# Optimization experiments

Measured on AMD Instinct MI355X. Metric: run time of the kernel, lower is better.

## Reference

```python
import jax, jax.numpy as jnp
import numpy as np

C_M, C_Z, H, C_HID = 256, 128, 8, 32
N_SEQ, N_RES = 64, 384
INF = 1e9
EPS = 1e-5


def layernorm(x, w, b):
    mu = jnp.mean(x, axis=-1, keepdims=True)
    var = jnp.mean(jnp.square(x - mu), axis=-1, keepdims=True)
    return (x - mu) * jax.lax.rsqrt(var + EPS) * w + b


def setup_inputs() -> dict:
    key = jax.random.key(0)
    ks = jax.random.split(key, 6)
    m = jax.random.normal(ks[0], (N_SEQ, N_RES, C_M), dtype=jnp.float32)
    z = jax.random.normal(ks[1], (N_RES, N_RES, C_Z), dtype=jnp.float32)
    mask = jnp.ones((N_SEQ, N_RES), dtype=jnp.float32)
    return {
        "m": m,
        "z": z,
        "mask": mask,
        "ln_m_w": jnp.ones((C_M,), jnp.float32),
        "ln_m_b": jnp.zeros((C_M,), jnp.float32),
        "ln_z_w": jnp.ones((C_Z,), jnp.float32),
        "ln_z_b": jnp.zeros((C_Z,), jnp.float32),
        "W_z": jax.random.normal(ks[2], (C_Z, H), jnp.float32) * 0.05,
        "W_v": jax.random.normal(ks[3], (C_M, H * C_HID), jnp.float32) * 0.05,
        "W_g": jax.random.normal(ks[4], (C_M, H * C_HID), jnp.float32) * 0.05,
        "W_o": jax.random.normal(ks[5], (H * C_HID, C_M), jnp.float32) * 0.05,
    }


def reference(m, z, mask, ln_m_w, ln_m_b, ln_z_w, ln_z_b, W_z, W_v, W_g, W_o):
    S, N = m.shape[0], m.shape[1]
    # mask: max over MSA rows, keepdim -> [1, N]; bias -> [1,1,1,N]
    mask_max = jnp.max(mask, axis=-2, keepdims=True)
    mask_bias = (INF * (mask_max - 1.0))[:, None, None, :]  # [1,1,1,N]
    # pair bias: LN(z) @ W_z -> [N,N,H] -> [H,N,N]
    zb = layernorm(z, ln_z_w, ln_z_b) @ W_z  # [N,N,H]
    zb = jnp.transpose(zb, (2, 0, 1))  # [H,N,N]
    # LN on m
    m_ln = layernorm(m, ln_m_w, ln_m_b)  # [S,N,C_m]
    # values: [S,N,H*c] -> [S,H,N,c]
    v = (m_ln @ W_v).reshape(S, N, H, C_HID).transpose(0, 2, 1, 3)
    # attention weights from summed biases (no QK): [1,H,N,N] after broadcast
    a = jax.nn.softmax(mask_bias + zb[None], axis=-1)  # [1,H,N,N]
    # o = a @ v  -> [S,H,N,c]
    o = jnp.einsum('hqk,shkc->shqc', a[0], v)
    o = o.transpose(0, 2, 1, 3)  # [S,N,H,c]
    # sigmoid gate
    g = jax.nn.sigmoid(m_ln @ W_g).reshape(S, N, H, C_HID)
    o = (o * g).reshape(S, N, H * C_HID)
    return o @ W_o  # [S,N,C_m]
```

## Files before the change

kernel.cpp:

```cpp
#include <hip/hip_runtime.h>
#include <math.h>

#define S 64
#define NRES 384
#define CM 256
#define CZ 128
#define NH 8
#define CH 32
#define HC 256

typedef unsigned short u16;
typedef __attribute__((ext_vector_type(8))) short bf16x8;
typedef __attribute__((ext_vector_type(4))) float f32x4;
typedef __attribute__((ext_vector_type(8))) unsigned short ushort8;
typedef __attribute__((ext_vector_type(4))) unsigned short ushort4_t;

#define OFF_BIAS 0
#define OFF_WT   200704
#define OFF_WOT  462848
#define OFF_A    593920
#define OFF_VT   2953216
#define OFF_G    15536128
#define OFF_O    28119040
#define OFF_MLN  40701952
#define OFF_ZB   OFF_O

__device__ __forceinline__ u16 f2bf(float f) {
    union { float f; unsigned int u; } v; v.f = f;
    unsigned int u = v.u;
    u += 0x7fff + ((u >> 16) & 1);
    return (u16)(u >> 16);
}
__device__ __forceinline__ float bf2f(u16 b) {
    union { float f; unsigned int u; } v; v.u = ((unsigned int)b) << 16;
    return v.f;
}
__device__ __forceinline__ void gload16(const u16* g, u16* l) {
    __builtin_amdgcn_global_load_lds(
        (const __attribute__((address_space(1))) void*)g,
        (__attribute__((address_space(3))) void*)l, 16, 0, 0);
}

__global__ __launch_bounds__(256) void k_stage1(
        const float* __restrict__ z, const float* __restrict__ Wz,
        const float* __restrict__ lzw, const float* __restrict__ lzb,
        const float* __restrict__ mask,
        const float* __restrict__ Wv, const float* __restrict__ Wg,
        const float* __restrict__ Wo, const float* __restrict__ m,
        const float* __restrict__ lmw, const float* __restrict__ lmb,
        float* __restrict__ zb, float* __restrict__ bias,
        u16* __restrict__ Wt, u16* __restrict__ Wot, u16* __restrict__ mln) {
    const int bid = blockIdx.x, tid = threadIdx.x;
    if (bid < 2304) {
        const int wave = tid >> 6, lane = tid & 63;
        const int rl = lane & 15, kg = lane >> 4;
        const int row0 = bid * 64 + wave * 16;
        const float* zrow = z + (size_t)(row0 + rl) * CZ + kg * 8;
        bf16x8 af[4];
        float sm = 0.f, sq = 0.f;
        #pragma unroll
        for (int t = 0; t < 4; ++t) {
            const float4 x0 = *(const float4*)&zrow[t * 32];
            const float4 x1 = *(const float4*)&zrow[t * 32 + 4];
            float xs[8] = {x0.x, x0.y, x0.z, x0.w, x1.x, x1.y, x1.z, x1.w};
            u16 tmp[8];
            #pragma unroll
            for (int e = 0; e < 8; ++e) {
                sm += xs[e]; sq += xs[e] * xs[e];
                tmp[e] = f2bf(xs[e]);
            }
            af[t] = *(bf16x8*)tmp;
        }
        sm += __shfl_xor(sm, 16); sq += __shfl_xor(sq, 16);
        sm += __shfl_xor(sm, 32); sq += __shfl_xor(sq, 32);
        const float mu = sm * (1.0f / CZ);
        const float var = sq * (1.0f / CZ) - mu * mu;
        const float rs = rsqrtf(var + 1e-5f);
        const int hh = lane & 7, seg = lane >> 3;
        float s1 = 0.f, s2 = 0.f;
        #pragma unroll
        for (int ci = 0; ci < 16; ++ci) {
            const int c = seg * 16 + ci;
            const float wz = Wz[c * NH + hh];
            s1 += lzw[c] * wz;
            s2 += lzb[c] * wz;
        }
        #pragma unroll
        for (int off = 8; off < 64; off <<= 1) {
            s1 += __shfl_xor(s1, off);
            s2 += __shfl_xor(s2, off);
        }
        bf16x8 bfr[4];
        #pragma unroll
        for (int t = 0; t < 4; ++t) {
            u16 tmp[8];
            #pragma unroll
            for (int e = 0; e < 8; ++e) {
                const int c = t * 32 + kg * 8 + e;
                tmp[e] = (rl < 8) ? f2bf(lzw[c] * Wz[c * NH + rl]) : (u16)0;
            }
            bfr[t] = *(bf16x8*)tmp;
        }
        f32x4 acc = {};
        #pragma unroll
        for (int t = 0; t < 4; ++t)
            acc = __builtin_amdgcn_mfma_f32_16x16x32_bf16(af[t], bfr[t], acc, 0, 0, 0);
        #pragma unroll
        for (int r = 0; r < 4; ++r) {
            const int rr = kg * 4 + r;
            const float mu_r = __shfl(mu, rr);
            const float rs_r = __shfl(rs, rr);
            const float p = rs_r * (acc[r] - mu_r * s1) + s2;
            if (rl < 8) zb[(size_t)(row0 + rr) * NH + rl] = p;
        }
    } else if (bid < 2306) {
        const int k = (bid - 2304) * 256 + tid;
        if (k < NRES) {
            float mx = -1e30f;
            for (int s = 0; s < S; ++s) mx = fmaxf(mx, mask[s * NRES + k]);
            bias[k] = 1e9f * (mx - 1.0f);
        }
    } else if (bid < 2818) {
        const int i = (bid - 2306) * 256 + tid;
        const int n = i >> 8, k = i & 255;
        const float v = (n < HC) ? Wv[(size_t)k * HC + n] : Wg[(size_t)k * HC + (n - HC)];
        Wt[i] = f2bf(v);
    } else if (bid < 3074) {
        const int i = (bid - 2818) * 256 + tid;
        const int n = i >> 8, k = i & 255;
        Wot[i] = f2bf(Wo[(size_t)k * CM + n]);
    } else {
        const int row = (bid - 3074) * 4 + (tid >> 6);
        const int lane = tid & 63;
        const float4 x = *(const float4*)&m[(size_t)row * CM + lane * 4];
        float sm = x.x + x.y + x.z + x.w;
        float sq = x.x*x.x + x.y*x.y + x.z*x.z + x.w*x.w;
        #pragma unroll
        for (int off = 32; off >= 1; off >>= 1) {
            sm += __shfl_xor(sm, off);
            sq += __shfl_xor(sq, off);
        }
        const float mu = sm * (1.0f / CM);
        const float var = sq * (1.0f / CM) - mu * mu;
        const float rs = rsqrtf(var + 1e-5f);
        const float4 w4 = *(const float4*)&lmw[lane * 4];
        const float4 b4 = *(const float4*)&lmb[lane * 4];
        u16 t4[4];
        t4[0] = f2bf((x.x - mu) * rs * w4.x + b4.x);
        t4[1] = f2bf((x.y - mu) * rs * w4.y + b4.y);
        t4[2] = f2bf((x.z - mu) * rs * w4.z + b4.z);
        t4[3] = f2bf((x.w - mu) * rs * w4.w + b4.w);
        *(ushort4_t*)&mln[(size_t)row * CM + lane * 4] = *(ushort4_t*)t4;
    }
}

__global__ __launch_bounds__(256) void k_stage2(
        const u16* __restrict__ mln, const u16* __restrict__ Wt,
        const float* __restrict__ zb, const float* __restrict__ bias,
        u16* __restrict__ vt, u16* __restrict__ g_, u16* __restrict__ a_out) {
    __shared__ u16 As[128][32];
    __shared__ u16 Bs[128][32];
    const int bid = blockIdx.x, tid = threadIdx.x;
    if (bid >= 768) {
        const int w = (bid - 768) * 4 + (tid >> 6);
        const int lane = tid & 63;
        const int h = w & 7, q = w >> 3;
        float v[6];
        float mx = -1e30f;
        #pragma unroll
        for (int t = 0; t < 6; ++t) {
            const int k = lane + 64 * t;
            v[t] = zb[((size_t)q * NRES + k) * NH + h] + bias[k];
            mx = fmaxf(mx, v[t]);
        }
        #pragma unroll
        for (int off = 32; off >= 1; off >>= 1) mx = fmaxf(mx, __shfl_xor(mx, off));
        float sum = 0.f;
        #pragma unroll
        for (int t = 0; t < 6; ++t) { v[t] = expf(v[t] - mx); sum += v[t]; }
        #pragma unroll
        for (int off = 32; off >= 1; off >>= 1) sum += __shfl_xor(sum, off);
        const float inv = 1.0f / sum;
        #pragma unroll
        for (int t = 0; t < 6; ++t)
            a_out[((size_t)h * NRES + q) * NRES + lane + 64 * t] = f2bf(v[t] * inv);
        return;
    }
    const int xcd = bid & 7, idx = bid >> 3;
    const int nt = idx & 3, mt = xcd * 24 + (idx >> 2);
    const int m0 = mt * 128, n0 = nt * 128;
    const int wave = tid >> 6, lane = tid & 63;
    const int wm = (wave >> 1) * 64, wn = (wave & 1) * 64;
    const int rl = lane & 15, kg = lane >> 4;
    const int lr = lane >> 2, lk = (lane & 3) * 8;
    const int wr = wave * 32;
    const u16* ag  = mln + (size_t)(m0 + wr + lr) * CM + lk;
    const u16* ag2 = ag + 16 * CM;
    const u16* bg  = Wt + (size_t)(n0 + wr + lr) * CM + lk;
    const u16* bg2 = bg + 16 * CM;
    u16* al  = &As[wr][0];
    u16* al2 = &As[wr + 16][0];
    u16* bl  = &Bs[wr][0];
    u16* bl2 = &Bs[wr + 16][0];
    const bool vhalf = (n0 < HC);
    f32x4 acc[4][4] = {};
    for (int kt = 0; kt < CM; kt += 32) {
        if (kt) __syncthreads();
        gload16(ag + kt, al);  gload16(ag2 + kt, al2);
        gload16(bg + kt, bl);  gload16(bg2 + kt, bl2);
        __syncthreads();
        bf16x8 af[4], bfr[4];
        #pragma unroll
        for (int i = 0; i < 4; ++i) af[i]  = *(const bf16x8*)&As[wm + i*16 + rl][kg*8];
        #pragma unroll
        for (int j = 0; j < 4; ++j) bfr[j] = *(const bf16x8*)&Bs[wn + j*16 + rl][kg*8];
        if (vhalf) {
            #pragma unroll
            for (int j = 0; j < 4; ++j)
                #pragma unroll
                for (int i = 0; i < 4; ++i)
                    acc[j][i] = __builtin_amdgcn_mfma_f32_16x16x32_bf16(bfr[j], af[i], acc[j][i], 0, 0, 0);
        } else {
            #pragma unroll
            for (int i = 0; i < 4; ++i)
                #pragma unroll
                for (int j = 0; j < 4; ++j)
                    acc[i][j] = __builtin_amdgcn_mfma_f32_16x16x32_bf16(af[i], bfr[j], acc[i][j], 0, 0, 0);
        }
    }
    if (vhalf) {
        #pragma unroll
        for (int j = 0; j < 4; ++j)
            #pragma unroll
            for (int r = 0; r < 4; ++r) {
                const int vcol = n0 + wn + j*16 + kg*4 + r;
                const int h = vcol >> 5, c = vcol & 31;
                #pragma unroll
                for (int i = 0; i < 4; ++i) {
                    const int mrowb = m0 + wm + i*16;
                    const int s = mrowb / NRES;
                    const int nn = mrowb - s * NRES + rl;
                    vt[(((size_t)h * S + s) * CH + c) * NRES + nn] = f2bf(acc[j][i][r]);
                }
            }
    } else {
        #pragma unroll
        for (int i = 0; i < 4; ++i)
            #pragma unroll
            for (int r = 0; r < 4; ++r) {
                const int row = m0 + wm + i*16 + kg*4 + r;
                #pragma unroll
                for (int j = 0; j < 4; ++j) {
                    const int gc = n0 + wn + j*16 + rl - HC;
                    g_[(size_t)row * HC + gc] = f2bf(1.0f / (1.0f + expf(-acc[i][j][r])));
                }
            }
    }
}

__global__ __launch_bounds__(256) void k_attn2(const u16* __restrict__ a_,
        const u16* __restrict__ vt, u16* __restrict__ o_) {
    __shared__ u16 As[128][32];
    __shared__ u16 Bs[128][32];
    const int tid = threadIdx.x;
    const int h = blockIdx.x & 7, rem = blockIdx.x >> 3;
    const int mt = rem >> 4, nt = rem & 15;
    const int q0 = mt * 128, sc0 = nt * 128;
    const int wave = tid >> 6, lane = tid & 63;
    const int wm = (wave >> 1) * 64, wn = (wave & 1) * 64;
    const int rl = lane & 15, kg = lane >> 4;
    const int lr = lane >> 2, lk = (lane & 3) * 8;
    const int wr = wave * 32;
    const u16* ag  = a_ + (size_t)h * NRES * NRES + (size_t)(q0 + wr + lr) * NRES + lk;
    const u16* ag2 = ag + 16 * NRES;
    const u16* bg  = vt + (size_t)h * S * CH * NRES + (size_t)(sc0 + wr + lr) * NRES + lk;
    const u16* bg2 = bg + 16 * NRES;
    u16* al  = &As[wr][0];
    u16* al2 = &As[wr + 16][0];
    u16* bl  = &Bs[wr][0];
    u16* bl2 = &Bs[wr + 16][0];
    f32x4 acc[4][4] = {};
    for (int kt = 0; kt < NRES; kt += 32) {
        if (kt) __syncthreads();
        gload16(ag + kt, al);  gload16(ag2 + kt, al2);
        gload16(bg + kt, bl);  gload16(bg2 + kt, bl2);
        __syncthreads();
        bf16x8 af[4], bfr[4];
        #pragma unroll
        for (int i = 0; i < 4; ++i) af[i]  = *(const bf16x8*)&As[wm + i*16 + rl][kg*8];
        #pragma unroll
        for (int j = 0; j < 4; ++j) bfr[j] = *(const bf16x8*)&Bs[wn + j*16 + rl][kg*8];
        #pragma unroll
        for (int i = 0; i < 4; ++i)
            #pragma unroll
            for (int j = 0; j < 4; ++j)
                acc[i][j] = __builtin_amdgcn_mfma_f32_16x16x32_bf16(af[i], bfr[j], acc[i][j], 0, 0, 0);
    }
    #pragma unroll
    for (int i = 0; i < 4; ++i)
        #pragma unroll
        for (int r = 0; r < 4; ++r) {
            const int q = q0 + wm + i*16 + kg*4 + r;
            #pragma unroll
            for (int j = 0; j < 4; ++j) {
                const int sc = sc0 + wn + j*16 + rl;
                const int s = sc >> 5, c = sc & 31;
                o_[(((size_t)s * NRES + q) * NH + h) * CH + c] = f2bf(acc[i][j][r]);
            }
        }
}

__global__ __launch_bounds__(256) void k_gemm_out(const u16* __restrict__ o_,
        const u16* __restrict__ g_, const u16* __restrict__ Wot,
        float* __restrict__ out) {
    __shared__ u16 As[128][40];
    __shared__ u16 Bs[128][32];
    const int tid = threadIdx.x;
    const int xcd = blockIdx.x & 7, idx = blockIdx.x >> 3;
    const int nt = idx & 1, mt = xcd * 24 + (idx >> 1);
    const int m0 = mt * 128, n0 = nt * 128;
    const int wave = tid >> 6, lane = tid & 63;
    const int wm = (wave >> 1) * 64, wn = (wave & 1) * 64;
    const int rl = lane & 15, kg = lane >> 4;
    const int lr = lane >> 2, lk = (lane & 3) * 8;
    const int wr = wave * 32;
    const int sr = tid >> 1, sh = (tid & 1) * 16;
    const u16* orow = o_ + (size_t)(m0 + sr) * HC;
    const u16* grow = g_ + (size_t)(m0 + sr) * HC;
    const u16* bg  = Wot + (size_t)(n0 + wr + lr) * HC + lk;
    const u16* bg2 = bg + 16 * HC;
    u16* bl  = &Bs[wr][0];
    u16* bl2 = &Bs[wr + 16][0];
    f32x4 acc[4][4] = {};
    for (int kt = 0; kt < HC; kt += 32) {
        if (kt) __syncthreads();
        gload16(bg + kt, bl);  gload16(bg2 + kt, bl2);
        {
            u16 tmp[16];
            const ushort8 ov0 = *(const ushort8*)&orow[kt + sh];
            const ushort8 ov1 = *(const ushort8*)&orow[kt + sh + 8];
            const ushort8 gv0 = *(const ushort8*)&grow[kt + sh];
            const ushort8 gv1 = *(const ushort8*)&grow[kt + sh + 8];
            #pragma unroll
            for (int p = 0; p < 8; ++p) {
                tmp[p]     = f2bf(bf2f(ov0[p]) * bf2f(gv0[p]));
                tmp[p + 8] = f2bf(bf2f(ov1[p]) * bf2f(gv1[p]));
            }
            *(ushort8*)&As[sr][sh]     = *(ushort8*)&tmp[0];
            *(ushort8*)&As[sr][sh + 8] = *(ushort8*)&tmp[8];
        }
        __syncthreads();
        bf16x8 af[4], bfr[4];
        #pragma unroll
        for (int i = 0; i < 4; ++i) af[i]  = *(const bf16x8*)&As[wm + i*16 + rl][kg*8];
        #pragma unroll
        for (int j = 0; j < 4; ++j) bfr[j] = *(const bf16x8*)&Bs[wn + j*16 + rl][kg*8];
        #pragma unroll
        for (int i = 0; i < 4; ++i)
            #pragma unroll
            for (int j = 0; j < 4; ++j)
                acc[i][j] = __builtin_amdgcn_mfma_f32_16x16x32_bf16(af[i], bfr[j], acc[i][j], 0, 0, 0);
    }
    #pragma unroll
    for (int i = 0; i < 4; ++i)
        #pragma unroll
        for (int r = 0; r < 4; ++r) {
            const int row = m0 + wm + i*16 + kg*4 + r;
            #pragma unroll
            for (int j = 0; j < 4; ++j)
                out[(size_t)row * CM + n0 + wn + j*16 + rl] = acc[i][j][r];
        }
}

extern "C" void kernel_launch(void* const* d_in, const int* in_sizes, int n_in,
                              void* d_out, int out_size, void* d_ws, size_t ws_size,
                              hipStream_t stream) {
    const float* m      = (const float*)d_in[0];
    const float* z      = (const float*)d_in[1];
    const float* mask   = (const float*)d_in[2];
    const float* ln_m_w = (const float*)d_in[3];
    const float* ln_m_b = (const float*)d_in[4];
    const float* ln_z_w = (const float*)d_in[5];
    const float* ln_z_b = (const float*)d_in[6];
    const float* Wz     = (const float*)d_in[7];
    const float* Wv     = (const float*)d_in[8];
    const float* Wg     = (const float*)d_in[9];
    const float* Wo     = (const float*)d_in[10];
    float* out = (float*)d_out;
    char* ws = (char*)d_ws;

    float* bias = (float*)(ws + OFF_BIAS);
    u16* Wt     = (u16*)(ws + OFF_WT);
    u16* Wot    = (u16*)(ws + OFF_WOT);
    u16* a      = (u16*)(ws + OFF_A);
    u16* vtw    = (u16*)(ws + OFF_VT);
    u16* gw     = (u16*)(ws + OFF_G);
    u16* ow     = (u16*)(ws + OFF_O);
    u16* mlnw   = (u16*)(ws + OFF_MLN);
    float* zbw  = (float*)(ws + OFF_ZB);

    k_stage1<<<9218, 256, 0, stream>>>(z, Wz, ln_z_w, ln_z_b, mask, Wv, Wg, Wo,
                                       m, ln_m_w, ln_m_b, zbw, bias, Wt, Wot, mlnw);
    k_stage2<<<1536, 256, 0, stream>>>(mlnw, Wt, zbw, bias, vtw, gw, a);
    k_attn2<<<384, 256, 0, stream>>>(a, vtw, ow);
    k_gemm_out<<<384, 256, 0, stream>>>(ow, gw, Wot, out);
}
```

Baseline: 85.00 us.

## Store pair bias head-major and amortize weight prep across two row tiles

```diff
diff --git a/kernel.cpp b/kernel.cpp
--- a/kernel.cpp
+++ b/kernel.cpp
@@ -8,6 +8,7 @@
 #define NH 8
 #define CH 32
 #define HC 256
+#define NROW 147456
 
 typedef unsigned short u16;
 typedef __attribute__((ext_vector_type(8))) short bf16x8;
@@ -51,86 +52,105 @@
         float* __restrict__ zb, float* __restrict__ bias,
         u16* __restrict__ Wt, u16* __restrict__ Wot, u16* __restrict__ mln) {
     const int bid = blockIdx.x, tid = threadIdx.x;
-    if (bid < 2304) {
+    if (bid < 1152) {
+        __shared__ u16 sWWT[16 * 128];
+        __shared__ float sPart[2][2][8];
         const int wave = tid >> 6, lane = tid & 63;
         const int rl = lane & 15, kg = lane >> 4;
-        const int row0 = bid * 64 + wave * 16;
-        const float* zrow = z + (size_t)(row0 + rl) * CZ + kg * 8;
-        bf16x8 af[4];
-        float sm = 0.f, sq = 0.f;
-        #pragma unroll
-        for (int t = 0; t < 4; ++t) {
-            const float4 x0 = *(const float4*)&zrow[t * 32];
-            const float4 x1 = *(const float4*)&zrow[t * 32 + 4];
-            float xs[8] = {x0.x, x0.y, x0.z, x0.w, x1.x, x1.y, x1.z, x1.w};
-            u16 tmp[8];
-            #pragma unroll
-            for (int e = 0; e < 8; ++e) {
-                sm += xs[e]; sq += xs[e] * xs[e];
-                tmp[e] = f2bf(xs[e]);
-            }
-            af[t] = *(bf16x8*)tmp;
-        }
-        sm += __shfl_xor(sm, 16); sq += __shfl_xor(sq, 16);
-        sm += __shfl_xor(sm, 32); sq += __shfl_xor(sq, 32);
-        const float mu = sm * (1.0f / CZ);
-        const float var = sq * (1.0f / CZ) - mu * mu;
-        const float rs = rsqrtf(var + 1e-5f);
-        const int hh = lane & 7, seg = lane >> 3;
-        float s1 = 0.f, s2 = 0.f;
-        #pragma unroll
-        for (int ci = 0; ci < 16; ++ci) {
-            const int c = seg * 16 + ci;
-            const float wz = Wz[c * NH + hh];
-            s1 += lzw[c] * wz;
-            s2 += lzb[c] * wz;
-        }
-        #pragma unroll
-        for (int off = 8; off < 64; off <<= 1) {
-            s1 += __shfl_xor(s1, off);
-            s2 += __shfl_xor(s2, off);
-        }
+        if (tid < 128) {
+            const int c = tid;
+            const float4 wz0 = *(const float4*)&Wz[c * 8];
+            const float4 wz1 = *(const float4*)&Wz[c * 8 + 4];
+            const float lw = lzw[c], lbv = lzb[c];
+            float wzv[8] = {wz0.x, wz0.y, wz0.z, wz0.w, wz1.x, wz1.y, wz1.z, wz1.w};
+            float ww[8], wb[8];
+            #pragma unroll
+            for (int h = 0; h < 8; ++h) {
+                ww[h] = lw * wzv[h];
+                wb[h] = lbv * wzv[h];
+                sWWT[h * 128 + c] = f2bf(ww[h]);
+                sWWT[(8 + h) * 128 + c] = 0;
+            }
+            #pragma unroll
+            for (int h = 0; h < 8; ++h) {
+                #pragma unroll
+                for (int off = 1; off < 64; off <<= 1) {
+                    ww[h] += __shfl_xor(ww[h], off);
+                    wb[h] += __shfl_xor(wb[h], off);
+                }
+            }
+            if (lane == 0) {
+                #pragma unroll
+                for (int h = 0; h < 8; ++h) {
+                    sPart[wave][0][h] = ww[h];
+                    sPart[wave][1][h] = wb[h];
+                }
+            }
+        }
+        __syncthreads();
+        const float c1 = (rl < 8) ? (sPart[0][0][rl] + sPart[1][0][rl]) : 0.f;
+        const float c2 = (rl < 8) ? (sPart[0][1][rl] + sPart[1][1][rl]) : 0.f;
         bf16x8 bfr[4];
         #pragma unroll
-        for (int t = 0; t < 4; ++t) {
-            u16 tmp[8];
-            #pragma unroll
-            for (int e = 0; e < 8; ++e) {
-                const int c = t * 32 + kg * 8 + e;
-                tmp[e] = (rl < 8) ? f2bf(lzw[c] * Wz[c * NH + rl]) : (u16)0;
-            }
-            bfr[t] = *(bf16x8*)tmp;
-        }
-        f32x4 acc = {};
-        #pragma unroll
         for (int t = 0; t < 4; ++t)
-            acc = __builtin_amdgcn_mfma_f32_16x16x32_bf16(af[t], bfr[t], acc, 0, 0, 0);
-        #pragma unroll
-        for (int r = 0; r < 4; ++r) {
-            const int rr = kg * 4 + r;
-            const float mu_r = __shfl(mu, rr);
-            const float rs_r = __shfl(rs, rr);
-            const float p = rs_r * (acc[r] - mu_r * s1) + s2;
-            if (rl < 8) zb[(size_t)(row0 + rr) * NH + rl] = p;
-        }
-    } else if (bid < 2306) {
-        const int k = (bid - 2304) * 256 + tid;
+            bfr[t] = *(const bf16x8*)&sWWT[rl * 128 + kg * 8 + t * 32];
+        #pragma unroll
+        for (int it = 0; it < 2; ++it) {
+            const int row0 = bid * 128 + it * 64 + wave * 16;
+            const float* zrow = z + (size_t)(row0 + rl) * CZ + kg * 8;
+            bf16x8 af[4];
+            float sm = 0.f, sq = 0.f;
+            #pragma unroll
+            for (int t = 0; t < 4; ++t) {
+                const float4 x0 = *(const float4*)&zrow[t * 32];
+                const float4 x1 = *(const float4*)&zrow[t * 32 + 4];
+                float xs[8] = {x0.x, x0.y, x0.z, x0.w, x1.x, x1.y, x1.z, x1.w};
+                u16 tmp[8];
+                #pragma unroll
+                for (int e = 0; e < 8; ++e) {
+                    sm += xs[e]; sq += xs[e] * xs[e];
+                    tmp[e] = f2bf(xs[e]);
+                }
+                af[t] = *(bf16x8*)tmp;
+            }
+            sm += __shfl_xor(sm, 16); sq += __shfl_xor(sq, 16);
+            sm += __shfl_xor(sm, 32); sq += __shfl_xor(sq, 32);
+            const float mu = sm * (1.0f / CZ);
+            const float var = sq * (1.0f / CZ) - mu * mu;
+            const float rs = rsqrtf(var + 1e-5f);
+            f32x4 acc = {};
+            #pragma unroll
+            for (int t = 0; t < 4; ++t)
+                acc = __builtin_amdgcn_mfma_f32_16x16x32_bf16(af[t], bfr[t], acc, 0, 0, 0);
+            f32x4 pv;
+            #pragma unroll
+            for (int r = 0; r < 4; ++r) {
+                const int rr = kg * 4 + r;
+                const float mu_r = __shfl(mu, rr);
+                const float rs_r = __shfl(rs, rr);
+                pv[r] = rs_r * (acc[r] - mu_r * c1) + c2;
+            }
+            if (rl < 8)
+                *(f32x4*)&zb[(size_t)rl * NROW + row0 + kg * 4] = pv;
+        }
+    } else if (bid < 1154) {
+        const int k = (bid - 1152) * 256 + tid;
         if (k < NRES) {
             float mx = -1e30f;
             for (int s = 0; s < S; ++s) mx = fmaxf(mx, mask[s * NRES + k]);
             bias[k] = 1e9f * (mx - 1.0f);
         }
-    } else if (bid < 2818) {
-        const int i = (bid - 2306) * 256 + tid;
+    } else if (bid < 1666) {
+        const int i = (bid - 1154) * 256 + tid;
         const int n = i >> 8, k = i & 255;
         const float v = (n < HC) ? Wv[(size_t)k * HC + n] : Wg[(size_t)k * HC + (n - HC)];
         Wt[i] = f2bf(v);
-    } else if (bid < 3074) {
-        const int i = (bid - 2818) * 256 + tid;
+    } else if (bid < 1922) {
+        const int i = (bid - 1666) * 256 + tid;
         const int n = i >> 8, k = i & 255;
         Wot[i] = f2bf(Wo[(size_t)k * CM + n]);
     } else {
-        const int row = (bid - 3074) * 4 + (tid >> 6);
+        const int row = (bid - 1922) * 4 + (tid >> 6);
         const int lane = tid & 63;
         const float4 x = *(const float4*)&m[(size_t)row * CM + lane * 4];
         float sm = x.x + x.y + x.z + x.w;
@@ -165,12 +185,13 @@
         const int w = (bid - 768) * 4 + (tid >> 6);
         const int lane = tid & 63;
         const int h = w & 7, q = w >> 3;
+        const float* zbh = zb + (size_t)h * NROW + (size_t)q * NRES;
         float v[6];
         float mx = -1e30f;
         #pragma unroll
         for (int t = 0; t < 6; ++t) {
             const int k = lane + 64 * t;
-            v[t] = zb[((size_t)q * NRES + k) * NH + h] + bias[k];
+            v[t] = zbh[k] + bias[k];
             mx = fmaxf(mx, v[t]);
         }
         #pragma unroll
@@ -399,7 +420,7 @@
     u16* mlnw   = (u16*)(ws + OFF_MLN);
     float* zbw  = (float*)(ws + OFF_ZB);
 
-    k_stage1<<<9218, 256, 0, stream>>>(z, Wz, ln_z_w, ln_z_b, mask, Wv, Wg, Wo,
+    k_stage1<<<8066, 256, 0, stream>>>(z, Wz, ln_z_w, ln_z_b, mask, Wv, Wg, Wo,
                                        m, ln_m_w, ln_m_b, zbw, bias, Wt, Wot, mlnw);
     k_stage2<<<1536, 256, 0, stream>>>(mlnw, Wt, zbw, bias, vtw, gw, a);
     k_attn2<<<384, 256, 0, stream>>>(a, vtw, ow);
```

After: 76.77 us. 9.7% less time.
